# Kernel optimization log

Measured on AMD Instinct MI355X. Metric: run time of the kernel, lower is better.

Reference implementation:

```python
import jax, jax.numpy as jnp
import numpy as np

B, H, N, D, W = 2, 12, 2048, 128, 64  # batch, heads, seq, head_dim (1536/12), nnz per row


def setup_inputs() -> dict:
    key = jax.random.key(0)
    kq, kk, kv, kc = jax.random.split(key, 4)
    q = jax.random.normal(kq, (B, H, N, D), jnp.float32)
    k = jax.random.normal(kk, (B, H, N, D), jnp.float32)
    v = jax.random.normal(kv, (B, H, N, D), jnp.float32)
    # CSR-style sparse attention topology: each query row attends to W columns,
    # column indices sorted within each row (as Sputnik requires).
    col_ids = jnp.sort(jax.random.randint(kc, (N, W), 0, N, dtype=jnp.int32), axis=-1)
    return {"q": q, "k": k, "v": v, "col_ids": col_ids}


def reference(q, k, v, col_ids):
    # SDDMM: scores only at sparse positions -> [B, H, N, W]
    scale = 1.0 / jnp.sqrt(jnp.float32(q.shape[-1]))
    kg = k[:, :, col_ids]  # gather K rows per sparse column: [B, H, N, W, D]
    scores = jnp.einsum('bhnd,bhnwd->bhnw', q, kg) * scale
    # Row-wise sparse softmax (fixed W nnz per row -> dense softmax over last axis)
    probs = jax.nn.softmax(scores, axis=-1)
    # SPMM: sparse probs @ V -> [B, H, N, D]
    vg = v[:, :, col_ids]  # [B, H, N, W, D]
    return jnp.einsum('bhnw,bhnwd->bhnd', probs, vg)
```

## Files before the change

kernel.cpp:

```cpp
#include <hip/hip_runtime.h>
#include <hip/hip_bf16.h>
#include <hip/hip_fp16.h>

constexpr int Bc = 2;
constexpr int Hc = 12;
constexpr int Nc = 2048;
constexpr int Dc = 128;
constexpr int Wc = 64;
constexpr float SCALE = 0.08838834764831845f;
constexpr int ELEMS = Bc * Hc * Nc * Dc;

typedef _Float16 h2v __attribute__((ext_vector_type(2)));

__device__ __forceinline__ unsigned packh2(float a, float b) {
    const __half2 h = __floats2half2_rn(a, b);
    return __builtin_bit_cast(unsigned, h);
}

__device__ __forceinline__ float dot2h(unsigned kp, unsigned qp, float acc) {
#if __has_builtin(__builtin_amdgcn_fdot2)
    return __builtin_amdgcn_fdot2(__builtin_bit_cast(h2v, kp),
                                  __builtin_bit_cast(h2v, qp), acc, false);
#else
    const float2 kf = __half22float2(__builtin_bit_cast(__half2, kp));
    const float2 qf = __half22float2(__builtin_bit_cast(__half2, qp));
    return acc + kf.x * qf.x + kf.y * qf.y;
#endif
}

__device__ __forceinline__ float2 h22f2(unsigned u) {
    return __half22float2(__builtin_bit_cast(__half2, u));
}

__global__ __launch_bounds__(256) void cvt_kernel(
    const float* __restrict__ k,
    const float* __restrict__ v,
    unsigned* __restrict__ kh,
    unsigned* __restrict__ vh)
{
    const int i = blockIdx.x * 256 + threadIdx.x;
    const float4 kk = ((const float4*)k)[i];
    const float4 vv = ((const float4*)v)[i];
    uint2 ko, vo;
    ko.x = packh2(kk.x, kk.y);  ko.y = packh2(kk.z, kk.w);
    vo.x = packh2(vv.x, vv.y);  vo.y = packh2(vv.z, vv.w);
    ((uint2*)kh)[i] = ko;
    ((uint2*)vh)[i] = vo;
}

__global__ __launch_bounds__(256) void sca_wave_kernel(
    const float* __restrict__ q,
    const unsigned short* __restrict__ kh,
    const unsigned short* __restrict__ vh,
    const int*   __restrict__ col_ids,
    float*       __restrict__ out)
{
    const int t    = threadIdx.x;
    const int wv   = t >> 6;
    const int lane = t & 63;

    const int i    = blockIdx.x;
    const int xcd  = i & 7;
    const int slot = i >> 3;
    const int hg   = slot % 3;
    const int nb   = slot / 3;
    const int bh   = xcd + 8 * hg;
    const int n    = nb * 4 + wv;
    const int row  = bh * Nc + n;

    const int c_own = col_ids[n * Wc + lane];

    const float*          qrow  = q  + (size_t)row * Dc;
    const unsigned short* kbase = kh + (size_t)bh * Nc * Dc;
    const unsigned short* vbase = vh + (size_t)bh * Nc * Dc;

    const int p8 = lane & 7;
    const int o8 = lane >> 3;
    const int g  = lane >> 4;
    const int j  = lane & 15;

    const float4* q4 = (const float4*)qrow;
    const float4 qa0 = q4[2 * p8];
    const float4 qa1 = q4[2 * p8 + 1];
    const float4 qb0 = q4[16 + 2 * p8];
    const float4 qb1 = q4[16 + 2 * p8 + 1];
    unsigned qp[8];
    qp[0] = packh2(qa0.x, qa0.y);  qp[1] = packh2(qa0.z, qa0.w);
    qp[2] = packh2(qa1.x, qa1.y);  qp[3] = packh2(qa1.z, qa1.w);
    qp[4] = packh2(qb0.x, qb0.y);  qp[5] = packh2(qb0.z, qb0.w);
    qp[6] = packh2(qb1.x, qb1.y);  qp[7] = packh2(qb1.z, qb1.w);

    float sc[8];
#pragma unroll
    for (int P = 0; P < 8; ++P) {
        const int cc = __shfl(c_own, 8 * P + o8);
        const uint4* krow = (const uint4*)(kbase + (size_t)cc * Dc);
        const uint4 k0 = krow[p8];
        const uint4 k1 = krow[8 + p8];
        float acc = 0.0f;
        acc = dot2h(k0.x, qp[0], acc);
        acc = dot2h(k0.y, qp[1], acc);
        acc = dot2h(k0.z, qp[2], acc);
        acc = dot2h(k0.w, qp[3], acc);
        acc = dot2h(k1.x, qp[4], acc);
        acc = dot2h(k1.y, qp[5], acc);
        acc = dot2h(k1.z, qp[6], acc);
        acc = dot2h(k1.w, qp[7], acc);
        acc += __shfl_xor(acc, 1);
        acc += __shfl_xor(acc, 2);
        acc += __shfl_xor(acc, 4);
        sc[P] = acc * SCALE;
    }

    float e[8];
    float s = 0.0f;
#pragma unroll
    for (int P = 0; P < 8; ++P) { e[P] = __expf(sc[P]); s += e[P]; }
#pragma unroll
    for (int off = 8; off < 64; off <<= 1) s += __shfl_xor(s, off);
    const float inv = 1.0f / s;
    float pn[8];
#pragma unroll
    for (int P = 0; P < 8; ++P) pn[P] = e[P] * inv;

    float4 accA = make_float4(0.f, 0.f, 0.f, 0.f);
    float4 accB = make_float4(0.f, 0.f, 0.f, 0.f);
#pragma unroll
    for (int ii = 0; ii < 16; ++ii) {
        const int cc = __shfl(c_own, 4 * ii + g);
        const float pr = __shfl(pn[ii >> 1], 32 * (ii & 1) + 8 * g);
        const uint4 vv = ((const uint4*)(vbase + (size_t)cc * Dc))[j];
        const float2 f0 = h22f2(vv.x);
        const float2 f1 = h22f2(vv.y);
        const float2 f2 = h22f2(vv.z);
        const float2 f3 = h22f2(vv.w);
        accA.x += pr * f0.x;  accA.y += pr * f0.y;
        accA.z += pr * f1.x;  accA.w += pr * f1.y;
        accB.x += pr * f2.x;  accB.y += pr * f2.y;
        accB.z += pr * f3.x;  accB.w += pr * f3.y;
    }
#pragma unroll
    for (int off = 16; off <= 32; off <<= 1) {
        accA.x += __shfl_xor(accA.x, off);
        accA.y += __shfl_xor(accA.y, off);
        accA.z += __shfl_xor(accA.z, off);
        accA.w += __shfl_xor(accA.w, off);
        accB.x += __shfl_xor(accB.x, off);
        accB.y += __shfl_xor(accB.y, off);
        accB.z += __shfl_xor(accB.z, off);
        accB.w += __shfl_xor(accB.w, off);
    }

    if (lane < 16) {
        float4* orow = (float4*)(out + (size_t)row * Dc);
        orow[2 * j]     = accA;
        orow[2 * j + 1] = accB;
    }
}

__global__ __launch_bounds__(256) void sca_kernel(
    const float* __restrict__ q,
    const float* __restrict__ k,
    const float* __restrict__ v,
    const int*   __restrict__ col_ids,
    float*       __restrict__ out)
{
    const int bid = blockIdx.x;
    const int n   = bid & (Nc - 1);
    const int bh  = bid >> 11;
    const int t   = threadIdx.x;

    __shared__ int   s_cols[Wc];
    __shared__ float s_scores[Wc];
    __shared__ float s_probs[Wc];
    __shared__ float s_red[8 * Dc];

    if (t < Wc) s_cols[t] = col_ids[n * Wc + t];

    const float* qrow  = q + ((size_t)bh * Nc + n) * Dc;
    const float* kbase = k + (size_t)bh * Nc * Dc;
    const float* vbase = v + (size_t)bh * Nc * Dc;

    __syncthreads();
    {
        const int w = t >> 2;
        const int p = t & 3;
        const int c = s_cols[w];
        const float4* krow = (const float4*)(kbase + (size_t)c * Dc);
        const float4* q4   = (const float4*)qrow;
        float acc = 0.0f;
#pragma unroll
        for (int i = 0; i < 8; ++i) {
            const float4 kk = krow[p + 4 * i];
            const float4 qq = q4[p + 4 * i];
            acc += kk.x * qq.x + kk.y * qq.y + kk.z * qq.z + kk.w * qq.w;
        }
        acc += __shfl_xor(acc, 1);
        acc += __shfl_xor(acc, 2);
        if (p == 0) s_scores[w] = acc * SCALE;
    }
    __syncthreads();
    if (t < 64) {
        const float sv = s_scores[t];
        float m = sv;
#pragma unroll
        for (int off = 32; off > 0; off >>= 1) m = fmaxf(m, __shfl_xor(m, off));
        const float e = __expf(sv - m);
        float l = e;
#pragma unroll
        for (int off = 32; off > 0; off >>= 1) l += __shfl_xor(l, off);
        s_probs[t] = e / l;
    }
    __syncthreads();
    {
        const int j = t & 31;
        const int g = t >> 5;
        float4 acc = make_float4(0.f, 0.f, 0.f, 0.f);
#pragma unroll
        for (int i = 0; i < 8; ++i) {
            const int w  = g * 8 + i;
            const float pr = s_probs[w];
            const int   c  = s_cols[w];
            const float4 vv = ((const float4*)(vbase + (size_t)c * Dc))[j];
            acc.x += pr * vv.x;
            acc.y += pr * vv.y;
            acc.z += pr * vv.z;
            acc.w += pr * vv.w;
        }
        ((float4*)s_red)[g * 32 + j] = acc;
    }
    __syncthreads();
    if (t < Dc) {
        float sv = 0.0f;
#pragma unroll
        for (int g = 0; g < 8; ++g) sv += s_red[g * Dc + t];
        out[((size_t)bh * Nc + n) * Dc + t] = sv;
    }
}

extern "C" void kernel_launch(void* const* d_in, const int* in_sizes, int n_in,
                              void* d_out, int out_size, void* d_ws, size_t ws_size,
                              hipStream_t stream) {
    const float* q       = (const float*)d_in[0];
    const float* k       = (const float*)d_in[1];
    const float* v       = (const float*)d_in[2];
    const int*   col_ids = (const int*)  d_in[3];
    float*       out     = (float*)d_out;

    const int n_rows = Bc * Hc * Nc;
    const size_t need = (size_t)2 * ELEMS * sizeof(unsigned short);

    if (ws_size >= need) {
        unsigned* khp = (unsigned*)d_ws;
        unsigned* vhp = khp + ELEMS / 2;
        cvt_kernel<<<dim3(ELEMS / 4 / 256), dim3(256), 0, stream>>>(k, v, khp, vhp);
        sca_wave_kernel<<<dim3(n_rows / 4), dim3(256), 0, stream>>>(
            q, (const unsigned short*)khp, (const unsigned short*)vhp, col_ids, out);
    } else {
        sca_kernel<<<dim3(n_rows), dim3(256), 0, stream>>>(q, k, v, col_ids, out);
    }
}
```

Before: 184.4 us.

## Prefetch V rows alongside K in score loop and accumulate PV in packed fp16

The V rows for each gathered column are now loaded in the same loop as the K rows, using the same lane-to-column mapping, so V memory latency overlaps the score computation instead of following the softmax. The PV product is accumulated with packed half2 FMAs in registers, then widened to float and reduced across lanes with shuffles. This drops the second shuffle-driven gather loop, but it raises register pressure and accumulates in fp16, which costs accuracy.

```diff
diff --git a/kernel.cpp b/kernel.cpp
--- a/kernel.cpp
+++ b/kernel.cpp
@@ -17,19 +17,19 @@
     return __builtin_bit_cast(unsigned, h);
 }
 
+__device__ __forceinline__ __half2 bc2(unsigned u) {
+    return __builtin_bit_cast(__half2, u);
+}
+
 __device__ __forceinline__ float dot2h(unsigned kp, unsigned qp, float acc) {
 #if __has_builtin(__builtin_amdgcn_fdot2)
     return __builtin_amdgcn_fdot2(__builtin_bit_cast(h2v, kp),
                                   __builtin_bit_cast(h2v, qp), acc, false);
 #else
-    const float2 kf = __half22float2(__builtin_bit_cast(__half2, kp));
-    const float2 qf = __half22float2(__builtin_bit_cast(__half2, qp));
+    const float2 kf = __half22float2(bc2(kp));
+    const float2 qf = __half22float2(bc2(qp));
     return acc + kf.x * qf.x + kf.y * qf.y;
 #endif
-}
-
-__device__ __forceinline__ float2 h22f2(unsigned u) {
-    return __half22float2(__builtin_bit_cast(__half2, u));
 }
 
 __global__ __launch_bounds__(256) void cvt_kernel(
@@ -76,8 +76,6 @@
 
     const int p8 = lane & 7;
     const int o8 = lane >> 3;
-    const int g  = lane >> 4;
-    const int j  = lane & 15;
 
     const float4* q4 = (const float4*)qrow;
     const float4 qa0 = q4[2 * p8];
@@ -91,12 +89,16 @@
     qp[6] = packh2(qb1.x, qb1.y);  qp[7] = packh2(qb1.z, qb1.w);
 
     float sc[8];
+    uint4 v0[8], v1[8];
 #pragma unroll
     for (int P = 0; P < 8; ++P) {
         const int cc = __shfl(c_own, 8 * P + o8);
-        const uint4* krow = (const uint4*)(kbase + (size_t)cc * Dc);
-        const uint4 k0 = krow[p8];
-        const uint4 k1 = krow[8 + p8];
+        const uint4* kr = (const uint4*)(kbase + (size_t)cc * Dc);
+        const uint4* vr = (const uint4*)(vbase + (size_t)cc * Dc);
+        const uint4 k0 = kr[p8];
+        const uint4 k1 = kr[8 + p8];
+        v0[P] = vr[p8];
+        v1[P] = vr[8 + p8];
         float acc = 0.0f;
         acc = dot2h(k0.x, qp[0], acc);
         acc = dot2h(k0.y, qp[1], acc);
@@ -111,50 +113,53 @@
         acc += __shfl_xor(acc, 4);
         sc[P] = acc * SCALE;
     }
-
-    float e[8];
+#if __has_builtin(__builtin_amdgcn_sched_barrier)
+    __builtin_amdgcn_sched_barrier(0);
+#endif
+
+    float pn[8];
     float s = 0.0f;
 #pragma unroll
-    for (int P = 0; P < 8; ++P) { e[P] = __expf(sc[P]); s += e[P]; }
+    for (int P = 0; P < 8; ++P) { pn[P] = __expf(sc[P]); s += pn[P]; }
 #pragma unroll
     for (int off = 8; off < 64; off <<= 1) s += __shfl_xor(s, off);
     const float inv = 1.0f / s;
-    float pn[8];
-#pragma unroll
-    for (int P = 0; P < 8; ++P) pn[P] = e[P] * inv;
-
-    float4 accA = make_float4(0.f, 0.f, 0.f, 0.f);
-    float4 accB = make_float4(0.f, 0.f, 0.f, 0.f);
-#pragma unroll
-    for (int ii = 0; ii < 16; ++ii) {
-        const int cc = __shfl(c_own, 4 * ii + g);
-        const float pr = __shfl(pn[ii >> 1], 32 * (ii & 1) + 8 * g);
-        const uint4 vv = ((const uint4*)(vbase + (size_t)cc * Dc))[j];
-        const float2 f0 = h22f2(vv.x);
-        const float2 f1 = h22f2(vv.y);
-        const float2 f2 = h22f2(vv.z);
-        const float2 f3 = h22f2(vv.w);
-        accA.x += pr * f0.x;  accA.y += pr * f0.y;
-        accA.z += pr * f1.x;  accA.w += pr * f1.y;
-        accB.x += pr * f2.x;  accB.y += pr * f2.y;
-        accB.z += pr * f3.x;  accB.w += pr * f3.y;
-    }
-#pragma unroll
-    for (int off = 16; off <= 32; off <<= 1) {
-        accA.x += __shfl_xor(accA.x, off);
-        accA.y += __shfl_xor(accA.y, off);
-        accA.z += __shfl_xor(accA.z, off);
-        accA.w += __shfl_xor(accA.w, off);
-        accB.x += __shfl_xor(accB.x, off);
-        accB.y += __shfl_xor(accB.y, off);
-        accB.z += __shfl_xor(accB.z, off);
-        accB.w += __shfl_xor(accB.w, off);
-    }
-
-    if (lane < 16) {
+
+    __half2 ah[8];
+#pragma unroll
+    for (int d = 0; d < 8; ++d) ah[d] = __floats2half2_rn(0.0f, 0.0f);
+#pragma unroll
+    for (int P = 0; P < 8; ++P) {
+        const float pr = pn[P] * inv;
+        const __half2 prh = __floats2half2_rn(pr, pr);
+        ah[0] = __hfma2(bc2(v0[P].x), prh, ah[0]);
+        ah[1] = __hfma2(bc2(v0[P].y), prh, ah[1]);
+        ah[2] = __hfma2(bc2(v0[P].z), prh, ah[2]);
+        ah[3] = __hfma2(bc2(v0[P].w), prh, ah[3]);
+        ah[4] = __hfma2(bc2(v1[P].x), prh, ah[4]);
+        ah[5] = __hfma2(bc2(v1[P].y), prh, ah[5]);
+        ah[6] = __hfma2(bc2(v1[P].z), prh, ah[6]);
+        ah[7] = __hfma2(bc2(v1[P].w), prh, ah[7]);
+    }
+    float f[16];
+#pragma unroll
+    for (int d = 0; d < 8; ++d) {
+        const float2 u = __half22float2(ah[d]);
+        f[2 * d]     = u.x;
+        f[2 * d + 1] = u.y;
+    }
+#pragma unroll
+    for (int off = 8; off < 64; off <<= 1) {
+#pragma unroll
+        for (int d = 0; d < 16; ++d) f[d] += __shfl_xor(f[d], off);
+    }
+
+    if (lane < 8) {
         float4* orow = (float4*)(out + (size_t)row * Dc);
-        orow[2 * j]     = accA;
-        orow[2 * j + 1] = accB;
+        orow[2 * p8]      = make_float4(f[0],  f[1],  f[2],  f[3]);
+        orow[2 * p8 + 1]  = make_float4(f[4],  f[5],  f[6],  f[7]);
+        orow[16 + 2 * p8] = make_float4(f[8],  f[9],  f[10], f[11]);
+        orow[17 + 2 * p8] = make_float4(f[12], f[13], f[14], f[15]);
     }
 }
 
```

Result: faster. 178.2 us (-3.4%).
